# Kernel optimization log

Hardware: AMD Instinct MI355X
Metric: run time of the kernel (lower is better)

Reference implementation:

```python
import jax, jax.numpy as jnp
import numpy as np

B, FC, FRAMES, C = 8, 256, 512, 256


def conv1d(x, w, stride=1, pad=(0, 0), dil=1):
    # x: [N, Cin, L], w: [Cout, Cin, K]
    return jax.lax.conv_general_dilated(
        x, w, window_strides=(stride,), padding=[pad],
        rhs_dilation=(dil,), dimension_numbers=('NCH', 'OIH', 'NCH'))


def setup_inputs() -> dict:
    key = jax.random.key(0)
    ks = jax.random.split(key, 8)
    s = 0.05
    x = jax.random.normal(ks[0], (B, FC, FRAMES), dtype=jnp.float32)
    enc_w0 = jax.random.normal(ks[1], (128, 1, 7), dtype=jnp.float32) * s
    enc_w123 = jax.random.normal(ks[2], (3, 128, 128, 7), dtype=jnp.float32) * s
    enc_w4567 = jax.random.normal(ks[3], (4, 128, 128, 3), dtype=jnp.float32) * s
    enc_w8 = jax.random.normal(ks[4], (C, 128, 1), dtype=jnp.float32) * s
    main_w = jax.random.normal(ks[5], (8, C, C, 2), dtype=jnp.float32) * s
    gate_w = jax.random.normal(ks[6], (8, C, C, 2), dtype=jnp.float32) * s
    judge_w = jax.random.normal(ks[7], (1, C, 1), dtype=jnp.float32) * s
    return {'x': x, 'enc_w0': enc_w0, 'enc_w123': enc_w123,
            'enc_w4567': enc_w4567, 'enc_w8': enc_w8,
            'main_w': main_w, 'gate_w': gate_w, 'judge_w': judge_w}


def reference(x, enc_w0, enc_w123, enc_w4567, enc_w8, main_w, gate_w, judge_w):
    lrelu = lambda h: jax.nn.leaky_relu(h, 0.2)
    b = x.shape[0]
    # [B, FC, FRAMES] -> [B*FRAMES, 1, FC]: encode each frame's feature vector
    h = jnp.transpose(x, (0, 2, 1)).reshape(-1, 1, FC)
    h = lrelu(conv1d(h, enc_w0, stride=2, pad=(3, 3)))
    for i in range(3):
        h = lrelu(conv1d(h, enc_w123[i], stride=2, pad=(3, 3)))
    for i in range(4):
        h = lrelu(conv1d(h, enc_w4567[i], stride=2, pad=(1, 1)))
    h = conv1d(h, enc_w8)                       # [B*FRAMES, C, 1], no activation
    h = jnp.transpose(h.reshape(b, FRAMES, C), (0, 2, 1))  # [B, C, FRAMES]
    # WaveNet stack: causal pad + dilated k=2 convs + tanh*sigmoid gate + residual
    feats = jnp.zeros_like(h)
    for i in range(8):
        p = 2 ** i
        z = jnp.tanh(conv1d(h, main_w[i], pad=(p, 0), dil=p)) * \
            jax.nn.sigmoid(conv1d(h, gate_w[i], pad=(p, 0), dil=p))
        feats = feats + z
        h = z + h                              # channels always match -> residual
    latent = feats
    j = conv1d(latent, judge_w)[:, :, -1:]      # [B, 1, 1]
    return latent[:, :, -1:], j
```

## Files before the change

### kernel.cpp

```cpp
#include <hip/hip_runtime.h>
#include <math.h>

#define FC 256
#define NB 8
#define RS 136

typedef __attribute__((ext_vector_type(8))) _Float16 f16x8;
typedef __attribute__((ext_vector_type(4))) float f32x4;

__device__ __forceinline__ float lrelu(float v) { return v > 0.f ? v : 0.2f * v; }
__device__ __forceinline__ unsigned short f2h(float f) {
  _Float16 h = (_Float16)f;
  return *(unsigned short*)&h;
}
__device__ __forceinline__ void bar() { asm volatile("s_barrier" ::: "memory"); }
__device__ __forceinline__ void wait_lgkm0() { asm volatile("s_waitcnt lgkmcnt(0)" ::: "memory"); }

#define N1 344064
#define N2 196608
#define N3 32768
#define NTOT 573440
#define NWN 2097152

__global__ void pack_kernel(const float* __restrict__ w123,
                            const float* __restrict__ w4567,
                            const float* __restrict__ w8,
                            const float* __restrict__ mw,
                            const float* __restrict__ gw,
                            unsigned short* __restrict__ wp,
                            unsigned short* __restrict__ wn) {
  int idx = blockIdx.x * 512 + threadIdx.x;
  if (idx < N1) {
    int e = idx & 7, lane = (idx >> 3) & 63, ct = (idx >> 9) & 7, ks = (idx >> 12) & 3, t = idx >> 14;
    int l = t / 7, kw = t % 7;
    int co = ct * 16 + (lane & 15), ci = ks * 32 + (lane >> 4) * 8 + e;
    wp[idx] = f2h(w123[(((l * 128 + co) * 128) + ci) * 7 + kw]);
  } else if (idx < N1 + N2) {
    int k = idx - N1;
    int e = k & 7, lane = (k >> 3) & 63, ct = (k >> 9) & 7, ks = (k >> 12) & 3, t = k >> 14;
    int l = t / 3, kw = t % 3;
    int co = ct * 16 + (lane & 15), ci = ks * 32 + (lane >> 4) * 8 + e;
    wp[idx] = f2h(w4567[(((l * 128 + co) * 128) + ci) * 3 + kw]);
  } else if (idx < NTOT) {
    int k = idx - N1 - N2;
    int e = k & 7, lane = (k >> 3) & 63, ct = (k >> 9) & 15, ks = (k >> 13) & 3;
    int co = ct * 16 + (lane & 15), ci = ks * 32 + (lane >> 4) * 8 + e;
    wp[idx] = f2h(w8[co * 128 + ci]);
  } else if (idx < NTOT + NWN) {
    int k2 = idx - NTOT;
    int li = k2 >> 18, w = k2 & 262143;
    int e = w & 7, lane = (w >> 3) & 63, rt = (w >> 9) & 31, k32 = w >> 14;
    int row = rt * 16 + (lane & 15), k = k32 * 32 + (lane >> 4) * 8 + e;
    int ch = row >> 1, mat = row & 1, kw = k >> 8, ci = k & 255;
    const float* src = mat ? gw : mw;
    wn[k2] = f2h(src[(((size_t)li * 256 + ch) * 256 + ci) * 2 + kw]);
  }
}

template<int KW, int POFF, int PIN, int POUT, int MC, int MN, int OM>
__device__ __forceinline__ void mlayer_d(const unsigned short* __restrict__ wp,
                                         const unsigned short* __restrict__ sin_,
                                         unsigned short* __restrict__ sout,
                                         unsigned short* __restrict__ gact,
                                         int tid, int frame) {
  constexpr int HRIN = PIN / 2 + 4;
  constexpr int HROUT = POUT / 2 + 4;
  constexpr int Nt = (POUT + 15) / 16;
  constexpr int MNg = Nt / MN;
  constexpr int MCg = 8 / MNg;
  static_assert(MC * MCg == 8, "cout tiling must cover 128 channels");
  constexpr int NS = KW * 4;
  constexpr int DA = NS < 4 ? NS : 4;
  constexpr int DB = NS < 3 ? NS : 3;

  const int wid = tid >> 6, lane = tid & 63, nl = lane & 15, q = lane >> 4;
  const int mcg = wid / MNg, mng = wid % MNg;
  const int ct0 = mcg * MC, nt0 = mng * MN;

  int jj[MN]; bool val[MN]; int rofs[MN][KW];
#pragma unroll
  for (int jn = 0; jn < MN; ++jn) {
    int n = (nt0 + jn) * 16 + nl;
    val[jn] = (n < POUT);
    jj[jn] = val[jn] ? n : 0;
#pragma unroll
    for (int kw = 0; kw < KW; ++kw) {
      int P = 2 * jj[jn] + kw - POFF + 4;
      rofs[jn][kw] = ((P & 1) * HRIN + (P >> 1)) * RS + q * 8;
    }
  }
  const unsigned short* wl = wp + (size_t)ct0 * 512 + lane * 8;

  f32x4 acc[MC][MN];
#pragma unroll
  for (int i = 0; i < MC; ++i)
#pragma unroll
    for (int jn = 0; jn < MN; ++jn) acc[i][jn] = (f32x4){0.f, 0.f, 0.f, 0.f};

  f16x8 A[DA][MC], B[DB][MN];
#pragma unroll
  for (int s = 0; s < DA; ++s)
#pragma unroll
    for (int i = 0; i < MC; ++i)
      A[s][i] = *(const f16x8*)(wl + (size_t)s * 4096 + i * 512);
#pragma unroll
  for (int s = 0; s < DB; ++s) {
    const int kw = s >> 2, ks = s & 3;
#pragma unroll
    for (int jn = 0; jn < MN; ++jn)
      B[s][jn] = *(const f16x8*)(sin_ + rofs[jn][kw] + ks * 32);
  }
#pragma unroll
  for (int s = 0; s < NS; ++s) {
    const int sa = s % DA, sb = s % DB;
#pragma unroll
    for (int i = 0; i < MC; ++i)
#pragma unroll
      for (int jn = 0; jn < MN; ++jn)
        acc[i][jn] = __builtin_amdgcn_mfma_f32_16x16x32_f16(A[sa][i], B[sb][jn], acc[i][jn], 0, 0, 0);
    if (s + DA < NS) {
#pragma unroll
      for (int i = 0; i < MC; ++i)
        A[sa][i] = *(const f16x8*)(wl + (size_t)(s + DA) * 4096 + i * 512);
    }
    if (s + DB < NS) {
      const int kw = (s + DB) >> 2, ks = (s + DB) & 3;
#pragma unroll
      for (int jn = 0; jn < MN; ++jn)
        B[sb][jn] = *(const f16x8*)(sin_ + rofs[jn][kw] + ks * 32);
    }
  }

#pragma unroll
  for (int i = 0; i < MC; ++i) {
#pragma unroll
    for (int jn = 0; jn < MN; ++jn) {
      if (!val[jn]) continue;
      unsigned int lo = (unsigned)f2h(lrelu(acc[i][jn][0])) | ((unsigned)f2h(lrelu(acc[i][jn][1])) << 16);
      unsigned int hi = (unsigned)f2h(lrelu(acc[i][jn][2])) | ((unsigned)f2h(lrelu(acc[i][jn][3])) << 16);
      const int j = jj[jn];
      if (OM == 1) {
        *(uint2*)(gact + ((size_t)frame * POUT + j) * 128 + (ct0 + i) * 16 + q * 4) = make_uint2(lo, hi);
      } else {
        const int row = (j & 1) * HROUT + (j >> 1) + 2;
        *(uint2*)(sout + (size_t)row * RS + (ct0 + i) * 16 + q * 4) = make_uint2(lo, hi);
      }
    }
  }
  if (OM == 0) {
    constexpr int DEND = ((POUT - 1) >> 1) + 3;
    constexpr int NZ = 2 + (HROUT - DEND);
    unsigned int* zp = (unsigned int*)sout;
    for (int s2 = tid; s2 < 2 * NZ * 68; s2 += 512) {
      int col = s2 % 68, rr = s2 / 68;
      int par = rr / NZ, rz = rr % NZ;
      int row = rz < 2 ? rz : DEND + rz - 2;
      zp[((size_t)par * HROUT + row) * 68 + col] = 0;
    }
    __syncthreads();
  }
}

__global__ __launch_bounds__(512, 4)
void encoder1(const float* __restrict__ x, const float* __restrict__ w0,
              const unsigned short* __restrict__ wp123,
              const unsigned short* __restrict__ wp4,
              unsigned short* __restrict__ act4g) {
  __shared__ __align__(16) unsigned short actA[18496];
  __shared__ __align__(16) unsigned short actB[9792];
  float* s_x = (float*)actB;
  const int tid = threadIdx.x;
  const int frame = blockIdx.x;
  const int bb = frame >> 8;
  const int t = (frame & 255) + 256;

  if (tid < 256) s_x[3 + tid] = x[((bb << 8) + tid) * 512 + t];
  else if (tid < 259) s_x[tid - 256] = 0.f;
  else if (tid < 262) s_x[tid] = 0.f;
  wait_lgkm0();
  bar();

  {
    const int c = tid & 127;
    const int half = tid >> 7;
    float wv[7];
#pragma unroll
    for (int k = 0; k < 7; ++k) wv[k] = w0[c * 7 + k];
    for (int j = half * 32; j < half * 32 + 32; ++j) {
      float s = 0.f;
#pragma unroll
      for (int k = 0; k < 7; ++k) s += wv[k] * s_x[2 * j + k];
      int row = ((j & 1) ? 68 : 0) + (j >> 1) + 2;
      actA[row * RS + c] = f2h(lrelu(s));
    }
    unsigned int* zp = (unsigned int*)actA;
    for (int s2 = tid; s2 < 2 * 4 * 68; s2 += 512) {
      int col = s2 % 68;
      int rr = s2 / 68;
      int par = rr >> 2, r2 = rr & 3;
      int row = (r2 < 2) ? r2 : (64 + r2);
      zp[((size_t)par * 68 + row) * 68 + col] = 0;
    }
  }
  wait_lgkm0();
  bar();

  mlayer_d<7, 3, 128, 64, 2, 2, 0>(wp123,          actA, actB, nullptr, tid, frame);
  mlayer_d<7, 3, 64, 32, 1, 2, 0>(wp123 + 114688,  actB, actA, nullptr, tid, frame);
  mlayer_d<7, 3, 32, 16, 1, 1, 0>(wp123 + 229376,  actA, actA + 5440, nullptr, tid, frame);
  mlayer_d<3, 1, 16, 8, 1, 1, 1>(wp4,              actA + 5440, nullptr, act4g, tid, frame);
}

template<int KW, int POFF, int PIN, int POUT, int FPB, int COUT, int MC, int MN, int OM, bool FLATIN>
__device__ __forceinline__ void mlayer(const unsigned short* __restrict__ wp,
                                       const unsigned short* __restrict__ sin_,
                                       unsigned short* __restrict__ sout,
                                       float* __restrict__ gout,
                                       int tid, int frame0) {
  constexpr int HRIN  = PIN / 2 + 4;
  constexpr int HROUT = POUT / 2 + 4;
  constexpr int NVAL = POUT * FPB;
  constexpr int Nt = (NVAL + 15) / 16;
  constexpr int Ct = COUT / 16;
  constexpr int MCg = Ct / MC, MNg = Nt / MN;
  constexpr int KS = 4;
  constexpr int NS = KW * KS;
  constexpr int DA = NS < 6 ? NS : 6;
  constexpr int DB = NS < 3 ? NS : 3;
  constexpr int L2P = POUT == 1 ? 0 : POUT == 2 ? 1 : POUT == 4 ? 2 : POUT == 8 ? 3 :
                      POUT == 16 ? 4 : POUT == 32 ? 5 : 6;

  const int wid = tid >> 6, lane = tid & 63, nl = lane & 15, q = lane >> 4;

  for (int mac = wid; mac < MCg * MNg; mac += 8) {
    const int mcg = mac / MNg, mng = mac % MNg;
    const int ct0 = mcg * MC, nt0 = mng * MN;
    int jj[MN]; bool val[MN];
#pragma unroll
    for (int jn = 0; jn < MN; ++jn) {
      int n = (nt0 + jn) * 16 + nl;
      val[jn] = (n < NVAL);
      jj[jn] = val[jn] ? n : 0;
    }
    int rofs[MN][KW];
#pragma unroll
    for (int jn = 0; jn < MN; ++jn) {
      const int f = jj[jn] >> L2P, j = jj[jn] & (POUT - 1);
#pragma unroll
      for (int kw = 0; kw < KW; ++kw) {
        if (FLATIN) {
          rofs[jn][kw] = jj[jn] * RS + q * 8;
        } else {
          int P = 2 * j + kw - POFF + 4;
          rofs[jn][kw] = (f * 2 * HRIN + (P & 1) * HRIN + (P >> 1)) * RS + q * 8;
        }
      }
    }
    int abase[MC];
#pragma unroll
    for (int i = 0; i < MC; ++i) abase[i] = (ct0 + i) * 512 + lane * 8;

    f32x4 acc[MC][MN];
#pragma unroll
    for (int i = 0; i < MC; ++i)
#pragma unroll
      for (int jn = 0; jn < MN; ++jn) acc[i][jn] = (f32x4){0.f, 0.f, 0.f, 0.f};

    f16x8 A[DA][MC], B[DB][MN];
#pragma unroll
    for (int s = 0; s < DA; ++s) {
      const int kw = s / KS, ks = s % KS;
#pragma unroll
      for (int i = 0; i < MC; ++i)
        A[s][i] = *(const f16x8*)(wp + (size_t)(kw * KS + ks) * (Ct * 512) + abase[i]);
    }
#pragma unroll
    for (int s = 0; s < DB; ++s) {
      const int kw = s / KS, ks = s % KS;
#pragma unroll
      for (int jn = 0; jn < MN; ++jn)
        B[s][jn] = *(const f16x8*)(sin_ + rofs[jn][kw] + ks * 32);
    }
#pragma unroll
    for (int s = 0; s < NS; ++s) {
      const int sa = s % DA, sb = s % DB;
#pragma unroll
      for (int i = 0; i < MC; ++i)
#pragma unroll
        for (int jn = 0; jn < MN; ++jn)
          acc[i][jn] = __builtin_amdgcn_mfma_f32_16x16x32_f16(A[sa][i], B[sb][jn], acc[i][jn], 0, 0, 0);
      if (s + DA < NS) {
        const int kw = (s + DA) / KS, ks = (s + DA) % KS;
#pragma unroll
        for (int i = 0; i < MC; ++i)
          A[sa][i] = *(const f16x8*)(wp + (size_t)(kw * KS + ks) * (Ct * 512) + abase[i]);
      }
      if (s + DB < NS) {
        const int kw = (s + DB) / KS, ks = (s + DB) % KS;
#pragma unroll
        for (int jn = 0; jn < MN; ++jn)
          B[sb][jn] = *(const f16x8*)(sin_ + rofs[jn][kw] + ks * 32);
      }
    }
#pragma unroll
    for (int i = 0; i < MC; ++i) {
#pragma unroll
      for (int jn = 0; jn < MN; ++jn) {
        if (OM == 3) {
          if (val[jn]) {
            const int frame = frame0 + jj[jn];
            float4 v = make_float4(acc[i][jn][0], acc[i][jn][1], acc[i][jn][2], acc[i][jn][3]);
            *(float4*)(gout + (size_t)frame * 256 + (ct0 + i) * 16 + q * 4) = v;
          }
        } else if (OM == 2) {
          if (val[jn]) {
            unsigned int lo = (unsigned)f2h(lrelu(acc[i][jn][0])) | ((unsigned)f2h(lrelu(acc[i][jn][1])) << 16);
            unsigned int hi = (unsigned)f2h(lrelu(acc[i][jn][2])) | ((unsigned)f2h(lrelu(acc[i][jn][3])) << 16);
            *(uint2*)(sout + (size_t)jj[jn] * RS + (ct0 + i) * 16 + q * 4) = make_uint2(lo, hi);
          }
        } else {
          if (val[jn]) {
            const int f = jj[jn] >> L2P, j = jj[jn] & (POUT - 1);
            const int row = f * 2 * HROUT + (j & 1) * HROUT + (j >> 1) + 2;
            unsigned int lo = (unsigned)f2h(lrelu(acc[i][jn][0])) | ((unsigned)f2h(lrelu(acc[i][jn][1])) << 16);
            unsigned int hi = (unsigned)f2h(lrelu(acc[i][jn][2])) | ((unsigned)f2h(lrelu(acc[i][jn][3])) << 16);
            *(uint2*)(sout + (size_t)row * RS + (ct0 + i) * 16 + q * 4) = make_uint2(lo, hi);
          }
        }
      }
    }
  }
  if (OM == 0) {
    constexpr int DEND = ((POUT - 1) >> 1) + 3;
    constexpr int NZ = 2 + (HROUT - DEND);
    constexpr int TOTU = FPB * 2 * NZ * (RS / 2);
    unsigned int* zp = (unsigned int*)sout;
    for (int s2 = tid; s2 < TOTU; s2 += 512) {
      int col = s2 % 68;
      int rr = s2 / 68;
      int fr = rr / (2 * NZ), r2 = rr % (2 * NZ);
      int par = r2 / NZ, rz = r2 % NZ;
      int row = rz < 2 ? rz : DEND + rz - 2;
      zp[((size_t)(fr * 2 + par) * HROUT + row) * 68 + col] = 0;
    }
    __syncthreads();
  } else if (OM == 2) {
    __syncthreads();
  }
}

__global__ __launch_bounds__(512)
void encoder2(const unsigned short* __restrict__ act4g,
              const unsigned short* __restrict__ wp4,
              const unsigned short* __restrict__ wp8,
              float* __restrict__ h) {
  __shared__ __align__(16) unsigned short actP[17408];
  __shared__ __align__(16) unsigned short actQ[13056];
  __shared__ __align__(16) unsigned short actR[2176];
  const int tid = threadIdx.x;
  const int frame0 = blockIdx.x * 8;

  {
    uint4 z4 = make_uint4(0, 0, 0, 0);
    for (int s = tid; s < 2176; s += 512) ((uint4*)actP)[s] = z4;
    for (int s = tid; s < 1632; s += 512) ((uint4*)actQ)[s] = z4;
    for (int s = tid; s < 272; s += 512) ((uint4*)actR)[s] = z4;
  }
  __syncthreads();
  for (int c = tid; c < 1024; c += 512) {
    int f = c >> 7, rem = c & 127, pos = rem >> 4, o = (rem & 15) * 8;
    uint4 v = *(const uint4*)(act4g + ((size_t)(frame0 + f) * 8 + pos) * 128 + o);
    int P = pos + 4;
    int row = (P & 1) * 8 + (P >> 1);
    *(uint4*)(actP + ((size_t)f * 16 + row) * RS + o) = v;
  }
  __syncthreads();

  mlayer<3, 1, 8, 4, 8, 128, 2, 1, 0, false>(wp4 + 49152,  actP, actQ, nullptr, tid, frame0);
  mlayer<3, 1, 4, 2, 8, 128, 1, 1, 0, false>(wp4 + 98304,  actQ, actP, nullptr, tid, frame0);
  mlayer<3, 1, 2, 1, 8, 128, 1, 1, 2, false>(wp4 + 147456, actP, actR, nullptr, tid, frame0);
  mlayer<1, 0, 1, 1, 8, 256, 1, 1, 3, true>(wp8,           actR, nullptr, h, tid, frame0);
}

__global__ __launch_bounds__(256)
void wnet_kernel(const unsigned short* __restrict__ wn,
                 const float* __restrict__ hsrc, float* __restrict__ hdst,
                 float* __restrict__ feats, int li, int init) {
  const int npos = 128 >> li, p = 1 << li, N = npos * 8, lnp = 7 - li;
  const int tid = threadIdx.x;
  const int nb = blockIdx.x >> 2, mb = blockIdx.x & 3;
  const int n0 = nb * 16;
  __shared__ __align__(16) unsigned short sB[16 * 520];

  for (int c = tid; c < 1024; c += 256) {
    const int nr = c >> 6, o = (c & 63) * 8;
    const int n = n0 + nr;
    unsigned short tmp[8] = {0, 0, 0, 0, 0, 0, 0, 0};
    if (n < N) {
      const int b = n >> lnp, kk = n & (npos - 1);
      const int t = 255 - (kk << (li + 1));
      const float* src = (o < 256) ? hsrc + ((size_t)(b * 256 + t - p)) * 256 + o
                                   : hsrc + ((size_t)(b * 256 + t)) * 256 + (o - 256);
#pragma unroll
      for (int e = 0; e < 8; ++e) tmp[e] = f2h(src[e]);
    }
    unsigned int u0 = (unsigned)tmp[0] | ((unsigned)tmp[1] << 16);
    unsigned int u1 = (unsigned)tmp[2] | ((unsigned)tmp[3] << 16);
    unsigned int u2 = (unsigned)tmp[4] | ((unsigned)tmp[5] << 16);
    unsigned int u3 = (unsigned)tmp[6] | ((unsigned)tmp[7] << 16);
    *(uint4*)(sB + (size_t)nr * 520 + o) = make_uint4(u0, u1, u2, u3);
  }
  __syncthreads();

  const int wid = tid >> 6, lane = tid & 63, nl = lane & 15, q = lane >> 4;
  f32x4 acc[2];
  acc[0] = (f32x4){0.f, 0.f, 0.f, 0.f};
  acc[1] = (f32x4){0.f, 0.f, 0.f, 0.f};
  int arow[2];
#pragma unroll
  for (int i = 0; i < 2; ++i) arow[i] = (mb * 8 + wid * 2 + i) * 512 + lane * 8;
  const int bofs = nl * 520 + q * 8;

  f16x8 A[4][2], Bv[2];
#pragma unroll
  for (int s = 0; s < 4; ++s)
#pragma unroll
    for (int i = 0; i < 2; ++i) A[s][i] = *(const f16x8*)(wn + arow[i] + (size_t)s * 16384);
#pragma unroll
  for (int s = 0; s < 2; ++s) Bv[s] = *(const f16x8*)(sB + bofs + s * 32);
#pragma unroll
  for (int s = 0; s < 16; ++s) {
    const int sa = s & 3, sb = s & 1;
    acc[0] = __builtin_amdgcn_mfma_f32_16x16x32_f16(A[sa][0], Bv[sb], acc[0], 0, 0, 0);
    acc[1] = __builtin_amdgcn_mfma_f32_16x16x32_f16(A[sa][1], Bv[sb], acc[1], 0, 0, 0);
    if (s + 4 < 16) {
#pragma unroll
      for (int i = 0; i < 2; ++i) A[sa][i] = *(const f16x8*)(wn + arow[i] + (size_t)(s + 4) * 16384);
    }
    if (s + 2 < 16) Bv[sb] = *(const f16x8*)(sB + bofs + (s + 2) * 32);
  }

  const int n = n0 + nl;
  if (n < N) {
    const int b = n >> lnp, kk = n & (npos - 1);
    const int t = 255 - (kk << (li + 1));
    const size_t rowoff = ((size_t)(b * 256 + t)) * 256;
#pragma unroll
    for (int i = 0; i < 2; ++i) {
      const int ch = mb * 64 + (wid * 2 + i) * 8 + q * 2;
      const float z0 = tanhf(acc[i][0]) * (1.f / (1.f + expf(-acc[i][1])));
      const float z1 = tanhf(acc[i][2]) * (1.f / (1.f + expf(-acc[i][3])));
      float2 hv = *(const float2*)(hsrc + rowoff + ch);
      *(float2*)(hdst + rowoff + ch) = make_float2(hv.x + z0, hv.y + z1);
      if (kk == 0) {
        float* fp = feats + b * 256 + ch;
        if (init) { fp[0] = z0; fp[1] = z1; }
        else { fp[0] += z0; fp[1] += z1; }
      }
    }
  }
}

template<int KC>
__global__ __launch_bounds__(256)
void wnet_partA(const unsigned short* __restrict__ wn,
                const float* __restrict__ hsrc,
                float* __restrict__ pb, int li) {
  const int npos = 128 >> li, p = 1 << li, N = npos * 8, lnp = 7 - li;
  const int NN = (N + 15) / 16;
  const int tid = threadIdx.x;
  int bid = blockIdx.x;
  const int mb = bid & 3; bid >>= 2;
  const int nb = bid % NN; const int ks = bid / NN;
  const int n0 = nb * 16;
  const int kc0 = ks * KC;
  constexpr int RSB = KC + 8;
  __shared__ __align__(16) unsigned short sB[16 * RSB];

  for (int c = tid; c < 2 * KC; c += 256) {
    const int nr = c / (KC / 8), oc = c % (KC / 8), o = oc * 8;
    const int kg = kc0 + o;
    const int n = n0 + nr;
    unsigned short tmp[8] = {0, 0, 0, 0, 0, 0, 0, 0};
    if (n < N) {
      const int b = n >> lnp, kk = n & (npos - 1);
      const int t = 255 - (kk << (li + 1));
      const float* src = (kg < 256) ? hsrc + ((size_t)(b * 256 + t - p)) * 256 + kg
                                    : hsrc + ((size_t)(b * 256 + t)) * 256 + (kg - 256);
#pragma unroll
      for (int e = 0; e < 8; ++e) tmp[e] = f2h(src[e]);
    }
    unsigned int u0 = (unsigned)tmp[0] | ((unsigned)tmp[1] << 16);
    unsigned int u1 = (unsigned)tmp[2] | ((unsigned)tmp[3] << 16);
    unsigned int u2 = (unsigned)tmp[4] | ((unsigned)tmp[5] << 16);
    unsigned int u3 = (unsigned)tmp[6] | ((unsigned)tmp[7] << 16);
    *(uint4*)(sB + (size_t)nr * RSB + o) = make_uint4(u0, u1, u2, u3);
  }
  __syncthreads();

  const int wid = tid >> 6, lane = tid & 63, nl = lane & 15, q = lane >> 4;
  f32x4 acc[2];
  acc[0] = (f32x4){0.f, 0.f, 0.f, 0.f};
  acc[1] = (f32x4){0.f, 0.f, 0.f, 0.f};
  int arow[2];
#pragma unroll
  for (int i = 0; i < 2; ++i)
    arow[i] = (((kc0 >> 5) * 32) + (mb * 8 + wid * 2 + i)) * 512 + lane * 8;
  const int bofs = nl * RSB + q * 8;

  constexpr int NS = KC / 32;
  constexpr int DA = NS < 4 ? NS : 4;
  constexpr int DB = NS < 2 ? NS : 2;
  f16x8 A[DA][2], Bv[DB];
#pragma unroll
  for (int s = 0; s < DA; ++s)
#pragma unroll
    for (int i = 0; i < 2; ++i) A[s][i] = *(const f16x8*)(wn + arow[i] + (size_t)s * 16384);
#pragma unroll
  for (int s = 0; s < DB; ++s) Bv[s] = *(const f16x8*)(sB + bofs + s * 32);
#pragma unroll
  for (int s = 0; s < NS; ++s) {
    const int sa = s % DA, sb = s % DB;
    acc[0] = __builtin_amdgcn_mfma_f32_16x16x32_f16(A[sa][0], Bv[sb], acc[0], 0, 0, 0);
    acc[1] = __builtin_amdgcn_mfma_f32_16x16x32_f16(A[sa][1], Bv[sb], acc[1], 0, 0, 0);
    if (s + DA < NS) {
#pragma unroll
      for (int i = 0; i < 2; ++i) A[sa][i] = *(const f16x8*)(wn + arow[i] + (size_t)(s + DA) * 16384);
    }
    if (s + DB < NS) Bv[sb] = *(const f16x8*)(sB + bofs + (s + DB) * 32);
  }
  float* base = pb + ((size_t)((ks * NN + nb) * 4 + mb) * 256 + tid) * 8;
  *(f32x4*)(base) = acc[0];
  *(f32x4*)(base + 4) = acc[1];
}

__global__ __launch_bounds__(256)
void wnet_partB(const float* __restrict__ pb,
                const float* __restrict__ hsrc, float* __restrict__ hdst,
                float* __restrict__ feats, int li, int ksplit) {
  const int npos = 128 >> li, N = npos * 8, lnp = 7 - li;
  const int NN = (N + 15) / 16;
  const int nb = blockIdx.x >> 2, mb = blockIdx.x & 3;
  const int n0 = nb * 16;
  const int tid = threadIdx.x;
  const int wid = tid >> 6, lane = tid & 63, nl = lane & 15, q = lane >> 4;
  float acc[8] = {0, 0, 0, 0, 0, 0, 0, 0};
  for (int ks = 0; ks < ksplit; ++ks) {
    const float* base = pb + ((size_t)((ks * NN + nb) * 4 + mb) * 256 + tid) * 8;
    float4 v0 = *(const float4*)(base);
    float4 v1 = *(const float4*)(base + 4);
    acc[0] += v0.x; acc[1] += v0.y; acc[2] += v0.z; acc[3] += v0.w;
    acc[4] += v1.x; acc[5] += v1.y; acc[6] += v1.z; acc[7] += v1.w;
  }
  const int n = n0 + nl;
  if (n < N) {
    const int b = n >> lnp, kk = n & (npos - 1);
    const int t = 255 - (kk << (li + 1));
    const size_t rowoff = ((size_t)(b * 256 + t)) * 256;
#pragma unroll
    for (int i = 0; i < 2; ++i) {
      const int ch = mb * 64 + (wid * 2 + i) * 8 + q * 2;
      const float z0 = tanhf(acc[i * 4 + 0]) * (1.f / (1.f + expf(-acc[i * 4 + 1])));
      const float z1 = tanhf(acc[i * 4 + 2]) * (1.f / (1.f + expf(-acc[i * 4 + 3])));
      float2 hv = *(const float2*)(hsrc + rowoff + ch);
      *(float2*)(hdst + rowoff + ch) = make_float2(hv.x + z0, hv.y + z1);
      if (kk == 0) {
        float* fp = feats + b * 256 + ch;
        fp[0] += z0; fp[1] += z1;
      }
    }
  }
}

__global__ void finalize_kernel(const float* __restrict__ feats,
                                const float* __restrict__ jw,
                                float* __restrict__ out) {
  __shared__ float red[256];
  const int b = blockIdx.x;
  const int tid = threadIdx.x;
  const float v = feats[b * 256 + tid];
  out[b * 256 + tid] = v;
  red[tid] = v * jw[tid];
  __syncthreads();
  for (int s = 128; s > 0; s >>= 1) {
    if (tid < s) red[tid] += red[tid + s];
    __syncthreads();
  }
  if (tid == 0) out[NB * 256 + b] = red[0];
}

extern "C" void kernel_launch(void* const* d_in, const int* in_sizes, int n_in,
                              void* d_out, int out_size, void* d_ws, size_t ws_size,
                              hipStream_t stream) {
  const float* x     = (const float*)d_in[0];
  const float* w0    = (const float*)d_in[1];
  const float* w123  = (const float*)d_in[2];
  const float* w4567 = (const float*)d_in[3];
  const float* w8    = (const float*)d_in[4];
  const float* mw    = (const float*)d_in[5];
  const float* gw    = (const float*)d_in[6];
  const float* jw    = (const float*)d_in[7];
  float* out = (float*)d_out;

  float* ws = (float*)d_ws;
  unsigned short* act4g = (unsigned short*)ws;
  float* h0    = ws + 1048576;
  float* h1    = ws + 1572864;
  float* feats = ws + 2097152;
  unsigned short* wp = (unsigned short*)(ws + 2099200);
  unsigned short* wn = (unsigned short*)(ws + 2385920);
  float* pb    = ws + 3434496;

  pack_kernel<<<5216, 512, 0, stream>>>(w123, w4567, w8, mw, gw, wp, wn);
  encoder1<<<2048, 512, 0, stream>>>(x, w0, wp, wp + N1, act4g);
  encoder2<<<256, 512, 0, stream>>>(act4g, wp + N1, wp + N1 + N2, h0);

  float* hs = h0; float* hd = h1;
  for (int i = 0; i < 8; ++i) {
    const unsigned short* wl = wn + (size_t)i * 262144;
    const int N = (128 >> i) * 8;
    const int nN = (N + 15) / 16;
    if (i < 2) {
      wnet_kernel<<<4 * nN, 256, 0, stream>>>(wl, hs, hd, feats, i, i == 0 ? 1 : 0);
    } else {
      int ksplit;
      if (i == 2)      { ksplit = 2;  wnet_partA<256><<<4 * nN * 2,  256, 0, stream>>>(wl, hs, pb, i); }
      else if (i == 3) { ksplit = 4;  wnet_partA<128><<<4 * nN * 4,  256, 0, stream>>>(wl, hs, pb, i); }
      else if (i == 4) { ksplit = 8;  wnet_partA<64> <<<4 * nN * 8,  256, 0, stream>>>(wl, hs, pb, i); }
      else             { ksplit = 16; wnet_partA<32> <<<4 * nN * 16, 256, 0, stream>>>(wl, hs, pb, i); }
      wnet_partB<<<4 * nN, 256, 0, stream>>>(pb, hs, hd, feats, i, ksplit);
    }
    float* tmp = hd; hd = hs; hs = tmp;
  }
  finalize_kernel<<<NB, 256, 0, stream>>>(feats, jw, out);
}
```

Before: 234.9 us.

## Fuse WaveNet layers and finalize into one cooperative kernel with grid sync

Replaces the per-layer WaveNet launches (including split-K partA/partB pairs) and the finalize kernel with a single cooperative kernel of 256 blocks. It loops over the 8 layers and uses grid.sync between them, then runs the judge reduction in the same kernel. The intent is to remove roughly 15 kernel launches and the partial-sum round trips through global memory. In exchange it drops split-K, so deep layers use few blocks, each doing the full K=512 reduction serially, and grid-wide barriers add their own cost.

```diff
diff --git a/kernel.cpp b/kernel.cpp
--- a/kernel.cpp
+++ b/kernel.cpp
@@ -1,5 +1,8 @@
 #include <hip/hip_runtime.h>
+#include <hip/hip_cooperative_groups.h>
 #include <math.h>
+
+namespace cg = cooperative_groups;
 
 #define FC 256
 #define NB 8
@@ -383,210 +386,110 @@
 }
 
 __global__ __launch_bounds__(256)
-void wnet_kernel(const unsigned short* __restrict__ wn,
-                 const float* __restrict__ hsrc, float* __restrict__ hdst,
-                 float* __restrict__ feats, int li, int init) {
-  const int npos = 128 >> li, p = 1 << li, N = npos * 8, lnp = 7 - li;
+void wnet_all(const unsigned short* __restrict__ wn,
+              float* __restrict__ h0, float* __restrict__ h1,
+              float* __restrict__ feats, const float* __restrict__ jw,
+              float* __restrict__ out) {
+  cg::grid_group grid = cg::this_grid();
   const int tid = threadIdx.x;
-  const int nb = blockIdx.x >> 2, mb = blockIdx.x & 3;
-  const int n0 = nb * 16;
+  const int blk = blockIdx.x;
+  const int wid = tid >> 6, lane = tid & 63, nl = lane & 15, q = lane >> 4;
   __shared__ __align__(16) unsigned short sB[16 * 520];
-
-  for (int c = tid; c < 1024; c += 256) {
-    const int nr = c >> 6, o = (c & 63) * 8;
-    const int n = n0 + nr;
-    unsigned short tmp[8] = {0, 0, 0, 0, 0, 0, 0, 0};
-    if (n < N) {
-      const int b = n >> lnp, kk = n & (npos - 1);
-      const int t = 255 - (kk << (li + 1));
-      const float* src = (o < 256) ? hsrc + ((size_t)(b * 256 + t - p)) * 256 + o
-                                   : hsrc + ((size_t)(b * 256 + t)) * 256 + (o - 256);
-#pragma unroll
-      for (int e = 0; e < 8; ++e) tmp[e] = f2h(src[e]);
-    }
-    unsigned int u0 = (unsigned)tmp[0] | ((unsigned)tmp[1] << 16);
-    unsigned int u1 = (unsigned)tmp[2] | ((unsigned)tmp[3] << 16);
-    unsigned int u2 = (unsigned)tmp[4] | ((unsigned)tmp[5] << 16);
-    unsigned int u3 = (unsigned)tmp[6] | ((unsigned)tmp[7] << 16);
-    *(uint4*)(sB + (size_t)nr * 520 + o) = make_uint4(u0, u1, u2, u3);
-  }
-  __syncthreads();
-
-  const int wid = tid >> 6, lane = tid & 63, nl = lane & 15, q = lane >> 4;
-  f32x4 acc[2];
-  acc[0] = (f32x4){0.f, 0.f, 0.f, 0.f};
-  acc[1] = (f32x4){0.f, 0.f, 0.f, 0.f};
-  int arow[2];
-#pragma unroll
-  for (int i = 0; i < 2; ++i) arow[i] = (mb * 8 + wid * 2 + i) * 512 + lane * 8;
-  const int bofs = nl * 520 + q * 8;
-
-  f16x8 A[4][2], Bv[2];
-#pragma unroll
-  for (int s = 0; s < 4; ++s)
-#pragma unroll
-    for (int i = 0; i < 2; ++i) A[s][i] = *(const f16x8*)(wn + arow[i] + (size_t)s * 16384);
-#pragma unroll
-  for (int s = 0; s < 2; ++s) Bv[s] = *(const f16x8*)(sB + bofs + s * 32);
-#pragma unroll
-  for (int s = 0; s < 16; ++s) {
-    const int sa = s & 3, sb = s & 1;
-    acc[0] = __builtin_amdgcn_mfma_f32_16x16x32_f16(A[sa][0], Bv[sb], acc[0], 0, 0, 0);
-    acc[1] = __builtin_amdgcn_mfma_f32_16x16x32_f16(A[sa][1], Bv[sb], acc[1], 0, 0, 0);
-    if (s + 4 < 16) {
-#pragma unroll
-      for (int i = 0; i < 2; ++i) A[sa][i] = *(const f16x8*)(wn + arow[i] + (size_t)(s + 4) * 16384);
-    }
-    if (s + 2 < 16) Bv[sb] = *(const f16x8*)(sB + bofs + (s + 2) * 32);
-  }
-
-  const int n = n0 + nl;
-  if (n < N) {
-    const int b = n >> lnp, kk = n & (npos - 1);
-    const int t = 255 - (kk << (li + 1));
-    const size_t rowoff = ((size_t)(b * 256 + t)) * 256;
-#pragma unroll
-    for (int i = 0; i < 2; ++i) {
-      const int ch = mb * 64 + (wid * 2 + i) * 8 + q * 2;
-      const float z0 = tanhf(acc[i][0]) * (1.f / (1.f + expf(-acc[i][1])));
-      const float z1 = tanhf(acc[i][2]) * (1.f / (1.f + expf(-acc[i][3])));
-      float2 hv = *(const float2*)(hsrc + rowoff + ch);
-      *(float2*)(hdst + rowoff + ch) = make_float2(hv.x + z0, hv.y + z1);
-      if (kk == 0) {
-        float* fp = feats + b * 256 + ch;
-        if (init) { fp[0] = z0; fp[1] = z1; }
-        else { fp[0] += z0; fp[1] += z1; }
-      }
-    }
-  }
-}
-
-template<int KC>
-__global__ __launch_bounds__(256)
-void wnet_partA(const unsigned short* __restrict__ wn,
-                const float* __restrict__ hsrc,
-                float* __restrict__ pb, int li) {
-  const int npos = 128 >> li, p = 1 << li, N = npos * 8, lnp = 7 - li;
-  const int NN = (N + 15) / 16;
-  const int tid = threadIdx.x;
-  int bid = blockIdx.x;
-  const int mb = bid & 3; bid >>= 2;
-  const int nb = bid % NN; const int ks = bid / NN;
-  const int n0 = nb * 16;
-  const int kc0 = ks * KC;
-  constexpr int RSB = KC + 8;
-  __shared__ __align__(16) unsigned short sB[16 * RSB];
-
-  for (int c = tid; c < 2 * KC; c += 256) {
-    const int nr = c / (KC / 8), oc = c % (KC / 8), o = oc * 8;
-    const int kg = kc0 + o;
-    const int n = n0 + nr;
-    unsigned short tmp[8] = {0, 0, 0, 0, 0, 0, 0, 0};
-    if (n < N) {
-      const int b = n >> lnp, kk = n & (npos - 1);
-      const int t = 255 - (kk << (li + 1));
-      const float* src = (kg < 256) ? hsrc + ((size_t)(b * 256 + t - p)) * 256 + kg
-                                    : hsrc + ((size_t)(b * 256 + t)) * 256 + (kg - 256);
-#pragma unroll
-      for (int e = 0; e < 8; ++e) tmp[e] = f2h(src[e]);
-    }
-    unsigned int u0 = (unsigned)tmp[0] | ((unsigned)tmp[1] << 16);
-    unsigned int u1 = (unsigned)tmp[2] | ((unsigned)tmp[3] << 16);
-    unsigned int u2 = (unsigned)tmp[4] | ((unsigned)tmp[5] << 16);
-    unsigned int u3 = (unsigned)tmp[6] | ((unsigned)tmp[7] << 16);
-    *(uint4*)(sB + (size_t)nr * RSB + o) = make_uint4(u0, u1, u2, u3);
-  }
-  __syncthreads();
-
-  const int wid = tid >> 6, lane = tid & 63, nl = lane & 15, q = lane >> 4;
-  f32x4 acc[2];
-  acc[0] = (f32x4){0.f, 0.f, 0.f, 0.f};
-  acc[1] = (f32x4){0.f, 0.f, 0.f, 0.f};
-  int arow[2];
-#pragma unroll
-  for (int i = 0; i < 2; ++i)
-    arow[i] = (((kc0 >> 5) * 32) + (mb * 8 + wid * 2 + i)) * 512 + lane * 8;
-  const int bofs = nl * RSB + q * 8;
-
-  constexpr int NS = KC / 32;
-  constexpr int DA = NS < 4 ? NS : 4;
-  constexpr int DB = NS < 2 ? NS : 2;
-  f16x8 A[DA][2], Bv[DB];
-#pragma unroll
-  for (int s = 0; s < DA; ++s)
-#pragma unroll
-    for (int i = 0; i < 2; ++i) A[s][i] = *(const f16x8*)(wn + arow[i] + (size_t)s * 16384);
-#pragma unroll
-  for (int s = 0; s < DB; ++s) Bv[s] = *(const f16x8*)(sB + bofs + s * 32);
-#pragma unroll
-  for (int s = 0; s < NS; ++s) {
-    const int sa = s % DA, sb = s % DB;
-    acc[0] = __builtin_amdgcn_mfma_f32_16x16x32_f16(A[sa][0], Bv[sb], acc[0], 0, 0, 0);
-    acc[1] = __builtin_amdgcn_mfma_f32_16x16x32_f16(A[sa][1], Bv[sb], acc[1], 0, 0, 0);
-    if (s + DA < NS) {
-#pragma unroll
-      for (int i = 0; i < 2; ++i) A[sa][i] = *(const f16x8*)(wn + arow[i] + (size_t)(s + DA) * 16384);
-    }
-    if (s + DB < NS) Bv[sb] = *(const f16x8*)(sB + bofs + (s + DB) * 32);
-  }
-  float* base = pb + ((size_t)((ks * NN + nb) * 4 + mb) * 256 + tid) * 8;
-  *(f32x4*)(base) = acc[0];
-  *(f32x4*)(base + 4) = acc[1];
-}
-
-__global__ __launch_bounds__(256)
-void wnet_partB(const float* __restrict__ pb,
-                const float* __restrict__ hsrc, float* __restrict__ hdst,
-                float* __restrict__ feats, int li, int ksplit) {
-  const int npos = 128 >> li, N = npos * 8, lnp = 7 - li;
-  const int NN = (N + 15) / 16;
-  const int nb = blockIdx.x >> 2, mb = blockIdx.x & 3;
-  const int n0 = nb * 16;
-  const int tid = threadIdx.x;
-  const int wid = tid >> 6, lane = tid & 63, nl = lane & 15, q = lane >> 4;
-  float acc[8] = {0, 0, 0, 0, 0, 0, 0, 0};
-  for (int ks = 0; ks < ksplit; ++ks) {
-    const float* base = pb + ((size_t)((ks * NN + nb) * 4 + mb) * 256 + tid) * 8;
-    float4 v0 = *(const float4*)(base);
-    float4 v1 = *(const float4*)(base + 4);
-    acc[0] += v0.x; acc[1] += v0.y; acc[2] += v0.z; acc[3] += v0.w;
-    acc[4] += v1.x; acc[5] += v1.y; acc[6] += v1.z; acc[7] += v1.w;
-  }
-  const int n = n0 + nl;
-  if (n < N) {
-    const int b = n >> lnp, kk = n & (npos - 1);
-    const int t = 255 - (kk << (li + 1));
-    const size_t rowoff = ((size_t)(b * 256 + t)) * 256;
-#pragma unroll
-    for (int i = 0; i < 2; ++i) {
-      const int ch = mb * 64 + (wid * 2 + i) * 8 + q * 2;
-      const float z0 = tanhf(acc[i * 4 + 0]) * (1.f / (1.f + expf(-acc[i * 4 + 1])));
-      const float z1 = tanhf(acc[i * 4 + 2]) * (1.f / (1.f + expf(-acc[i * 4 + 3])));
-      float2 hv = *(const float2*)(hsrc + rowoff + ch);
-      *(float2*)(hdst + rowoff + ch) = make_float2(hv.x + z0, hv.y + z1);
-      if (kk == 0) {
-        float* fp = feats + b * 256 + ch;
-        fp[0] += z0; fp[1] += z1;
-      }
-    }
-  }
-}
-
-__global__ void finalize_kernel(const float* __restrict__ feats,
-                                const float* __restrict__ jw,
-                                float* __restrict__ out) {
-  __shared__ float red[256];
-  const int b = blockIdx.x;
-  const int tid = threadIdx.x;
-  const float v = feats[b * 256 + tid];
-  out[b * 256 + tid] = v;
-  red[tid] = v * jw[tid];
-  __syncthreads();
-  for (int s = 128; s > 0; s >>= 1) {
-    if (tid < s) red[tid] += red[tid + s];
+  float* hs = h0; float* hd = h1;
+
+  for (int li = 0; li < 8; ++li) {
+    const int npos = 128 >> li, p = 1 << li, N = npos * 8, lnp = 7 - li;
+    const int nN = (N + 15) >> 4;
+    const unsigned short* wl = wn + (size_t)li * 262144;
+
+    if (blk < 4 * nN) {
+      const int nb = blk >> 2, mb = blk & 3;
+      const int n0 = nb * 16;
+      for (int c = tid; c < 1024; c += 256) {
+        const int nr = c >> 6, o = (c & 63) * 8;
+        const int n = n0 + nr;
+        unsigned short tmp[8] = {0, 0, 0, 0, 0, 0, 0, 0};
+        if (n < N) {
+          const int b = n >> lnp, kk = n & (npos - 1);
+          const int t = 255 - (kk << (li + 1));
+          const float* src = (o < 256) ? hs + ((size_t)(b * 256 + t - p)) * 256 + o
+                                       : hs + ((size_t)(b * 256 + t)) * 256 + (o - 256);
+#pragma unroll
+          for (int e = 0; e < 8; ++e) tmp[e] = f2h(src[e]);
+        }
+        unsigned int u0 = (unsigned)tmp[0] | ((unsigned)tmp[1] << 16);
+        unsigned int u1 = (unsigned)tmp[2] | ((unsigned)tmp[3] << 16);
+        unsigned int u2 = (unsigned)tmp[4] | ((unsigned)tmp[5] << 16);
+        unsigned int u3 = (unsigned)tmp[6] | ((unsigned)tmp[7] << 16);
+        *(uint4*)(sB + (size_t)nr * 520 + o) = make_uint4(u0, u1, u2, u3);
+      }
+      __syncthreads();
+
+      f32x4 acc[2];
+      acc[0] = (f32x4){0.f, 0.f, 0.f, 0.f};
+      acc[1] = (f32x4){0.f, 0.f, 0.f, 0.f};
+      int arow[2];
+#pragma unroll
+      for (int i = 0; i < 2; ++i) arow[i] = (mb * 8 + wid * 2 + i) * 512 + lane * 8;
+      const int bofs = nl * 520 + q * 8;
+
+      f16x8 A[4][2], Bv[2];
+#pragma unroll
+      for (int s = 0; s < 4; ++s)
+#pragma unroll
+        for (int i = 0; i < 2; ++i) A[s][i] = *(const f16x8*)(wl + arow[i] + (size_t)s * 16384);
+#pragma unroll
+      for (int s = 0; s < 2; ++s) Bv[s] = *(const f16x8*)(sB + bofs + s * 32);
+#pragma unroll
+      for (int s = 0; s < 16; ++s) {
+        const int sa = s & 3, sb = s & 1;
+        acc[0] = __builtin_amdgcn_mfma_f32_16x16x32_f16(A[sa][0], Bv[sb], acc[0], 0, 0, 0);
+        acc[1] = __builtin_amdgcn_mfma_f32_16x16x32_f16(A[sa][1], Bv[sb], acc[1], 0, 0, 0);
+        if (s + 4 < 16) {
+#pragma unroll
+          for (int i = 0; i < 2; ++i) A[sa][i] = *(const f16x8*)(wl + arow[i] + (size_t)(s + 4) * 16384);
+        }
+        if (s + 2 < 16) Bv[sb] = *(const f16x8*)(sB + bofs + (s + 2) * 32);
+      }
+
+      const int n = n0 + nl;
+      if (n < N) {
+        const int b = n >> lnp, kk = n & (npos - 1);
+        const int t = 255 - (kk << (li + 1));
+        const size_t rowoff = ((size_t)(b * 256 + t)) * 256;
+#pragma unroll
+        for (int i = 0; i < 2; ++i) {
+          const int ch = mb * 64 + (wid * 2 + i) * 8 + q * 2;
+          const float z0 = tanhf(acc[i][0]) * (1.f / (1.f + expf(-acc[i][1])));
+          const float z1 = tanhf(acc[i][2]) * (1.f / (1.f + expf(-acc[i][3])));
+          float2 hv = *(const float2*)(hs + rowoff + ch);
+          *(float2*)(hd + rowoff + ch) = make_float2(hv.x + z0, hv.y + z1);
+          if (kk == 0) {
+            float* fp = feats + b * 256 + ch;
+            if (li == 0) { fp[0] = z0; fp[1] = z1; }
+            else         { fp[0] += z0; fp[1] += z1; }
+          }
+        }
+      }
+      __syncthreads();
+    }
+    __threadfence();
+    grid.sync();
+    float* tsw = hs; hs = hd; hd = tsw;
+  }
+
+  if (blk < NB) {
+    float* red = (float*)sB;
+    const float v = feats[blk * 256 + tid];
+    out[blk * 256 + tid] = v;
+    red[tid] = v * jw[tid];
     __syncthreads();
-  }
-  if (tid == 0) out[NB * 256 + b] = red[0];
+    for (int s = 128; s > 0; s >>= 1) {
+      if (tid < s) red[tid] += red[tid + s];
+      __syncthreads();
+    }
+    if (tid == 0) out[NB * 256 + blk] = red[0];
+  }
 }
 
 extern "C" void kernel_launch(void* const* d_in, const int* in_sizes, int n_in,
@@ -609,28 +512,14 @@
   float* feats = ws + 2097152;
   unsigned short* wp = (unsigned short*)(ws + 2099200);
   unsigned short* wn = (unsigned short*)(ws + 2385920);
-  float* pb    = ws + 3434496;
 
   pack_kernel<<<5216, 512, 0, stream>>>(w123, w4567, w8, mw, gw, wp, wn);
   encoder1<<<2048, 512, 0, stream>>>(x, w0, wp, wp + N1, act4g);
   encoder2<<<256, 512, 0, stream>>>(act4g, wp + N1, wp + N1 + N2, h0);
 
-  float* hs = h0; float* hd = h1;
-  for (int i = 0; i < 8; ++i) {
-    const unsigned short* wl = wn + (size_t)i * 262144;
-    const int N = (128 >> i) * 8;
-    const int nN = (N + 15) / 16;
-    if (i < 2) {
-      wnet_kernel<<<4 * nN, 256, 0, stream>>>(wl, hs, hd, feats, i, i == 0 ? 1 : 0);
-    } else {
-      int ksplit;
-      if (i == 2)      { ksplit = 2;  wnet_partA<256><<<4 * nN * 2,  256, 0, stream>>>(wl, hs, pb, i); }
-      else if (i == 3) { ksplit = 4;  wnet_partA<128><<<4 * nN * 4,  256, 0, stream>>>(wl, hs, pb, i); }
-      else if (i == 4) { ksplit = 8;  wnet_partA<64> <<<4 * nN * 8,  256, 0, stream>>>(wl, hs, pb, i); }
-      else             { ksplit = 16; wnet_partA<32> <<<4 * nN * 16, 256, 0, stream>>>(wl, hs, pb, i); }
-      wnet_partB<<<4 * nN, 256, 0, stream>>>(pb, hs, hd, feats, i, ksplit);
-    }
-    float* tmp = hd; hd = hs; hs = tmp;
-  }
-  finalize_kernel<<<NB, 256, 0, stream>>>(feats, jw, out);
-}
+  const unsigned short* wnc = wn;
+  const float* jwc = jw;
+  void* kargs[] = {(void*)&wnc, (void*)&h0, (void*)&h1,
+                   (void*)&feats, (void*)&jwc, (void*)&out};
+  hipLaunchCooperativeKernel((void*)wnet_all, dim3(256), dim3(256), kargs, 0, stream);
+}
```

Result: slower. 619.6 us (+163.8%).
